# Optimization experiments

Hardware: AMD Instinct MI355X
Metric: run time of the kernel (lower is better)

The kernel has to match this reference:

```python
import jax, jax.numpy as jnp
import numpy as np
from jax import lax

PAD_TOKEN = 1
VOCAB = 32000
HID = 512
B, T, M = 32, 512, 6


def setup_inputs() -> dict:
    key = jax.random.key(0)
    ks = jax.random.split(key, 12)
    lim_g = 1.0 / np.sqrt(HID)
    lim_w = 1.0 / np.sqrt(2 * HID)
    u = lambda k, shape, lim: jax.random.uniform(k, shape, jnp.float32, -lim, lim)
    inp = {
        "input_seqs": jax.random.randint(ks[0], (B, T, M), 0, VOCAB, dtype=jnp.int32),
        "input_lengths": jax.random.randint(ks[1], (B,), 1, T + 1, dtype=jnp.int32),
        "emb": jax.random.normal(ks[2], (VOCAB, HID), jnp.float32),
        # forward GRU cell (Keras GRUCell, reset_after=True)
        "k_f": u(ks[3], (HID, 3 * HID), lim_g),
        "rk_f": u(ks[4], (HID, 3 * HID), lim_g),
        "b_f": u(ks[5], (2, 3 * HID), lim_g),
        # backward GRU cell
        "k_b": u(ks[6], (HID, 3 * HID), lim_g),
        "rk_b": u(ks[7], (HID, 3 * HID), lim_g),
        "b_b": u(ks[8], (2, 3 * HID), lim_g),
        # output projection W: 2H -> H
        "Wk": u(ks[9], (2 * HID, HID), lim_w),
        "Wb": u(ks[10], (HID,), lim_w),
    }
    return inp


def _gru_dir(x, mask, kernel, rkernel, bias, reverse):
    """Masked GRU scan. x: [B,T,H], mask: [B,T] bool. Keras GRUCell (reset_after=True).
    Masked timesteps carry previous state/output through (Keras semantics)."""
    b_in, b_rec = bias[0], bias[1]
    xs = x @ kernel + b_in                      # [B,T,3H], precompute input GEMM
    xs_t = jnp.swapaxes(xs, 0, 1)               # [T,B,3H]
    m_t = jnp.swapaxes(mask, 0, 1)              # [T,B]
    h0 = jnp.zeros((x.shape[0], rkernel.shape[0]), x.dtype)

    def step(h, inp):
        xt, mt = inp
        inner = h @ rkernel + b_rec             # [B,3H]
        xz, xr, xh = jnp.split(xt, 3, axis=-1)
        iz, ir, ih = jnp.split(inner, 3, axis=-1)
        z = jax.nn.sigmoid(xz + iz)
        r = jax.nn.sigmoid(xr + ir)
        hh = jnp.tanh(xh + r * ih)
        hn = z * h + (1.0 - z) * hh
        hn = jnp.where(mt[:, None], hn, h)      # masked step: carry state
        return hn, hn

    hT, outs = lax.scan(step, h0, (xs_t, m_t), reverse=reverse)
    return jnp.swapaxes(outs, 0, 1), hT         # [B,T,H], [B,H]


def reference(input_seqs, input_lengths, emb, k_f, rk_f, b_f, k_b, rk_b, b_b, Wk, Wb):
    # embedding lookup + PAD masking, sum over memory-tuple axis
    e = emb[input_seqs]                                       # [B,T,M,H]
    pad_mask = (input_seqs != PAD_TOKEN).astype(e.dtype)      # [B,T,M]
    embedded = jnp.sum(e * pad_mask[..., None], axis=2)       # [B,T,H]
    # (dropout p=0.0 -> identity)

    time_mask = jnp.arange(T)[None, :] < input_lengths[:, None]  # [B,T] bool

    out_f, h_f = _gru_dir(embedded, time_mask, k_f, rk_f, b_f, reverse=False)
    out_b, h_b = _gru_dir(embedded, time_mask, k_b, rk_b, b_b, reverse=True)

    outputs = jnp.concatenate([out_f, out_b], axis=-1)        # [B,T,2H]
    hidden_hat = jnp.concatenate([h_f, h_b], axis=-1)         # [B,2H]

    hidden = hidden_hat @ Wk + Wb                             # [B,H]
    outputs = outputs @ Wk + Wb                               # [B,T,H]
    return outputs, hidden
```

## Files before the change

### kernel.cpp

```cpp
#include <hip/hip_runtime.h>

typedef _Float16 f16;
typedef f16  f16x8 __attribute__((ext_vector_type(8)));
typedef float f32x4 __attribute__((ext_vector_type(4)));
typedef unsigned int u32;
typedef unsigned short u16;

#define NB   32
#define NT   512
#define NM   6
#define NH   512
#define NH3  1536
#define PADTOK 1
#define LO_SCALE 4096.0f
#define LO_INV   (1.0f/4096.0f)

#define XS2F_OFF  33685504
#define XS2B_OFF  100794368
#define HB_OFF    167903232
#define SLOT_STRIDE 544
#define FLAGS_U32 (2 * 32 * SLOT_STRIDE)
#define PLANE_E   16384

__device__ __forceinline__ void coh_store_u16(u16* base, u32 voff, u32 val) {
  asm volatile("global_store_short %0, %1, %2 sc0 sc1"
               :: "v"(voff), "v"(val), "s"(base) : "memory");
}

__global__ __launch_bounds__(128) void k_embed(const int* __restrict__ seqs,
                                               const float* __restrict__ emb,
                                               f16* __restrict__ Ahi,
                                               f16* __restrict__ Alo,
                                               f16* __restrict__ A2,
                                               u32* __restrict__ flags) {
  int row = blockIdx.x;
  int tid = threadIdx.x;
  if (row < 32) {
    for (int c2 = tid; c2 < 1024; c2 += 128)
      A2[(size_t)(16416 + row) * 1024 + c2] = (f16)0.f;
  }
  if (row < 64) {
    for (int j = row * 128 + tid; j < FLAGS_U32; j += 64 * 128)
      flags[j] = 0u;
  }
  const int* tr = seqs + (size_t)row * NM;
  int c0 = tid * 4;
  float acc0 = 0.f, acc1 = 0.f, acc2 = 0.f, acc3 = 0.f;
  for (int m = 0; m < NM; m++) {
    int tk = tr[m];
    if (tk != PADTOK) {
      float4 ev = *(const float4*)(emb + (size_t)tk * NH + c0);
      acc0 += ev.x; acc1 += ev.y; acc2 += ev.z; acc3 += ev.w;
    }
  }
  float a[4] = {acc0, acc1, acc2, acc3};
  for (int j = 0; j < 4; j++) {
    float v = a[j];
    f16 h = (f16)v;
    float lo = (v - (float)h) * LO_SCALE;
    Ahi[(size_t)row * NH + c0 + j] = h;
    Alo[(size_t)row * NH + c0 + j] = (f16)lo;
  }
}

__global__ __launch_bounds__(256) void k_gemm_in(const f16* __restrict__ Ahi,
                                                 const f16* __restrict__ Alo,
                                                 const float* __restrict__ Bw,
                                                 const float* __restrict__ bias,
                                                 f16* __restrict__ xs2) {
  __shared__ f16 BsH[64][40];
  __shared__ f16 BsL[64][40];
  int bx = blockIdx.x, by = blockIdx.y;
  int tid = threadIdx.x;
  int w = tid >> 6, l = tid & 63;
  int row0 = bx * 64 + w * 16;
  int col0 = by * 64;
  int arow = row0 + (l & 15);
  int kg = (l >> 4) * 8;
  f32x4 acc[4], accs[4];
  for (int nt = 0; nt < 4; nt++) {
    float bv = bias[col0 + nt * 16 + (l & 15)];
    f32x4 t = {bv, bv, bv, bv};
    acc[nt] = t;
    f32x4 z = {0.f, 0.f, 0.f, 0.f};
    accs[nt] = z;
  }
  for (int kb = 0; kb < NH; kb += 32) {
    __syncthreads();
    for (int idx = tid; idx < 2048; idx += 256) {
      int n = idx & 63, kl = idx >> 6;
      float v = Bw[(size_t)(kb + kl) * NH3 + col0 + n];
      f16 h = (f16)v;
      BsH[n][kl] = h;
      BsL[n][kl] = (f16)((v - (float)h) * LO_SCALE);
    }
    __syncthreads();
    f16x8 ah = *(const f16x8*)(Ahi + (size_t)arow * NH + kb + kg);
    f16x8 al = *(const f16x8*)(Alo + (size_t)arow * NH + kb + kg);
    for (int nt = 0; nt < 4; nt++) {
      f16x8 bh = *(const f16x8*)(&BsH[nt * 16 + (l & 15)][kg]);
      f16x8 bl = *(const f16x8*)(&BsL[nt * 16 + (l & 15)][kg]);
      acc[nt]  = __builtin_amdgcn_mfma_f32_16x16x32_f16(ah, bh, acc[nt], 0, 0, 0);
      accs[nt] = __builtin_amdgcn_mfma_f32_16x16x32_f16(al, bh, accs[nt], 0, 0, 0);
      accs[nt] = __builtin_amdgcn_mfma_f32_16x16x32_f16(ah, bl, accs[nt], 0, 0, 0);
    }
  }
  for (int nt = 0; nt < 4; nt++)
    for (int r = 0; r < 4; r++) {
      int grow = row0 + (l >> 4) * 4 + r;
      int b = grow >> 9, t = grow & (NT - 1);
      int gcol = col0 + nt * 16 + (l & 15);
      int g = gcol >> 9, u = gcol & 511;
      int ss = u >> 4, cc = u & 15;
      float v = acc[nt][r] + accs[nt][r] * LO_INV;
      f16 h = (f16)v;
      size_t idx = (size_t)(t * 32 + ss) * 2048 + g * 512 + b * 16 + cc;
      xs2[idx] = h;
      if (g == 2)
        xs2[idx + 512] = (f16)(v - (float)h);
    }
}

__global__ __launch_bounds__(128) void k_recur(const f16* __restrict__ xs2_f,
                                               const f16* __restrict__ xs2_b,
                                               const float* __restrict__ rk_f,
                                               const float* __restrict__ rk_b,
                                               const float* __restrict__ b_f,
                                               const float* __restrict__ b_b,
                                               const int* __restrict__ lens,
                                               u16* __restrict__ hb_f,
                                               u16* __restrict__ hb_b,
                                               f16* __restrict__ A2,
                                               u32* __restrict__ flags,
                                               int ring_mask) {
  __shared__ f16 WsH[48 * 512];
  __shared__ f16 WsL[48 * 512];
  int wg = blockIdx.x;
  int d = wg >> 5;
  int s = wg & 31;
  int u0 = s * 16;
  int tid = threadIdx.x;
  int w = tid >> 6, l = tid & 63;
  const f16*   xs2 = d ? xs2_b : xs2_f;
  u16*         myhb = d ? hb_b : hb_f;
  const float* rk = d ? rk_b : rk_f;
  const float* bb = d ? b_b  : b_f;

  for (int idx = tid; idx < 48 * 512; idx += 128) {
    int k = idx / 48, n = idx % 48;
    int gcol = (n >> 4) * NH + u0 + (n & 15);
    float v = rk[(size_t)k * NH3 + gcol];
    f16 h = (f16)v;
    f16 lo = (f16)((v - (float)h) * LO_SCALE);
    int byte = (n * 1024 + k * 2) ^ ((n & 7) << 4);
    *(f16*)((char*)WsH + byte) = h;
    *(f16*)((char*)WsL + byte) = lo;
  }
  __syncthreads();

  int c = l & 15;
  float brz = bb[NH3 + 0 * NH + u0 + c];
  float brr = bb[NH3 + 1 * NH + u0 + c];
  float brh = bb[NH3 + 2 * NH + u0 + c];
  int mrow[4], lenv[4];
  float hstate[4];
  u32 vo_h[4];
  for (int r = 0; r < 4; r++) {
    int b = w * 16 + (l >> 4) * 4 + r;
    mrow[r] = b;
    lenv[r] = lens[b];
    hstate[r] = 0.f;
    vo_h[r] = (u32)(s * 1024 + b * 32 + c * 2);
  }
  const int fbase = (d * 32 + s) * SLOT_STRIDE;
  for (int r = 0; r < 4; r++)
    coh_store_u16(myhb, vo_h[r], 0u);
  asm volatile("s_waitcnt vmcnt(0)" ::: "memory");
  __syncthreads();
  if (tid == 0)
    __hip_atomic_store(&flags[fbase + 0], 1u,
                       __ATOMIC_RELAXED, __HIP_MEMORY_SCOPE_AGENT);

  int arow_b = w * 16 + (l & 15);
  int kg = (l >> 4) * 8;
  int cbase = c * 1024;
  int zc = (c & 7) << 4;
  int hbase_lane = (kg >> 4) * 1024 + arow_b * 32 + (kg & 15) * 2;

#pragma unroll 1
  for (int i = 0; i < NT; i++) {
    int t = d ? (NT - 1 - i) : i;
    const u16* hplane = myhb + (size_t)(i & ring_mask) * PLANE_E;
    u16* wplane = myhb + (size_t)((i + 1) & ring_mask) * PLANE_E;

    if (tid < 32) {
      const u32* fp = flags + (d * 32 + tid) * SLOT_STRIDE + i;
      while (__hip_atomic_load(fp, __ATOMIC_RELAXED, __HIP_MEMORY_SCOPE_AGENT) == 0u)
        __builtin_amdgcn_s_sleep(1);
    }
    __syncthreads();

    const u16* sl = (const u16*)(xs2 + (size_t)(t * 32 + s) * 2048);
    u16 rxz[4], rxr[4], rxh[4], rxl[4];
#pragma unroll
    for (int r = 0; r < 4; r++) {
      int bo = mrow[r] * 16 + c;
      rxz[r] = sl[bo];
      rxr[r] = sl[512 + bo];
      rxh[r] = sl[1024 + bo];
      rxl[r] = sl[1536 + bo];
    }

    f32x4 a0, a1, a2, s0, s1, s2;
#pragma unroll
    for (int r = 0; r < 4; r++) {
      a0[r] = 0.f; a1[r] = 0.f; a2[r] = 0.f;
      s0[r] = 0.f; s1[r] = 0.f; s2[r] = 0.f;
    }
#pragma unroll
    for (int kk = 0; kk < 16; kk++) {
      f16x8 ah = *(const f16x8*)((const char*)hplane + hbase_lane + kk * 2048);
      int kb2 = (kk * 32 + kg) * 2;
      int off = (cbase + kb2) ^ zc;
      f16x8 b0h = *(const f16x8*)((const char*)WsH + off);
      f16x8 b1h = *(const f16x8*)((const char*)WsH + 16384 + off);
      f16x8 b2h = *(const f16x8*)((const char*)WsH + 32768 + off);
      f16x8 b0l = *(const f16x8*)((const char*)WsL + off);
      f16x8 b1l = *(const f16x8*)((const char*)WsL + 16384 + off);
      f16x8 b2l = *(const f16x8*)((const char*)WsL + 32768 + off);
      a0 = __builtin_amdgcn_mfma_f32_16x16x32_f16(ah, b0h, a0, 0, 0, 0);
      s0 = __builtin_amdgcn_mfma_f32_16x16x32_f16(ah, b0l, s0, 0, 0, 0);
      a1 = __builtin_amdgcn_mfma_f32_16x16x32_f16(ah, b1h, a1, 0, 0, 0);
      s1 = __builtin_amdgcn_mfma_f32_16x16x32_f16(ah, b1l, s1, 0, 0, 0);
      a2 = __builtin_amdgcn_mfma_f32_16x16x32_f16(ah, b2h, a2, 0, 0, 0);
      s2 = __builtin_amdgcn_mfma_f32_16x16x32_f16(ah, b2l, s2, 0, 0, 0);
    }

#pragma unroll
    for (int r = 0; r < 4; r++) {
      union { u16 u; f16 f; } uz, ur, uh, ul;
      uz.u = rxz[r]; ur.u = rxr[r]; uh.u = rxh[r]; ul.u = rxl[r];
      float az = a0[r] + s0[r] * LO_INV + (float)uz.f + brz;
      float ar = a1[r] + s1[r] * LO_INV + (float)ur.f + brr;
      float ahg = a2[r] + s2[r] * LO_INV;
      float xh = (float)uh.f + (float)ul.f;
      float z  = 1.f / (1.f + __expf(-az));
      float rr = 1.f / (1.f + __expf(-ar));
      float hh = tanhf(xh + rr * (ahg + brh));
      float hn = z * hstate[r] + (1.f - z) * hh;
      bool msk = t < lenv[r];
      hn = msk ? hn : hstate[r];
      hstate[r] = hn;
      union { f16 f; u16 u; } chv;
      chv.f = (f16)hn;
      coh_store_u16(wplane, vo_h[r], (u32)chv.u);
    }
    asm volatile("s_waitcnt vmcnt(0)" ::: "memory");
    __syncthreads();
    if (tid == 0)
      __hip_atomic_store(&flags[fbase + i + 1], 1u,
                         __ATOMIC_RELAXED, __HIP_MEMORY_SCOPE_AGENT);
#pragma unroll
    for (int r = 0; r < 4; r++)
      A2[((size_t)mrow[r] * NT + t) * 1024 + d * NH + u0 + c] = (f16)hstate[r];
  }
  for (int r = 0; r < 4; r++)
    A2[(size_t)(16384 + mrow[r]) * 1024 + d * NH + u0 + c] = (f16)hstate[r];
}

__global__ __launch_bounds__(256) void k_gemm_out(const f16* __restrict__ A2,
                                                  const float* __restrict__ Wk,
                                                  const float* __restrict__ Wb,
                                                  float* __restrict__ Out) {
  __shared__ f16 Bs[64][40];
  int bx = blockIdx.x, by = blockIdx.y;
  int tid = threadIdx.x;
  int w = tid >> 6, l = tid & 63;
  int row0 = bx * 64 + w * 16;
  int col0 = by * 64;
  int arow = row0 + (l & 15);
  int kg = (l >> 4) * 8;
  f32x4 acc[4];
  for (int nt = 0; nt < 4; nt++) {
    float bv = Wb[col0 + nt * 16 + (l & 15)];
    f32x4 t = {bv, bv, bv, bv};
    acc[nt] = t;
  }
  for (int kb = 0; kb < 1024; kb += 32) {
    __syncthreads();
    for (int idx = tid; idx < 2048; idx += 256) {
      int n = idx & 63, kl = idx >> 6;
      Bs[n][kl] = (f16)Wk[(size_t)(kb + kl) * NH + col0 + n];
    }
    __syncthreads();
    f16x8 av = *(const f16x8*)(A2 + (size_t)arow * 1024 + kb + kg);
    for (int nt = 0; nt < 4; nt++) {
      f16x8 bv = *(const f16x8*)(&Bs[nt * 16 + (l & 15)][kg]);
      acc[nt] = __builtin_amdgcn_mfma_f32_16x16x32_f16(av, bv, acc[nt], 0, 0, 0);
    }
  }
  for (int nt = 0; nt < 4; nt++)
    for (int r = 0; r < 4; r++) {
      int grow = row0 + (l >> 4) * 4 + r;
      if (grow < 16416)
        Out[(size_t)grow * NH + col0 + nt * 16 + (l & 15)] = acc[nt][r];
    }
}

extern "C" void kernel_launch(void* const* d_in, const int* in_sizes, int n_in,
                              void* d_out, int out_size, void* d_ws, size_t ws_size,
                              hipStream_t stream) {
  (void)in_sizes; (void)n_in; (void)out_size;
  const int*   seqs = (const int*)d_in[0];
  const int*   lens = (const int*)d_in[1];
  const float* emb  = (const float*)d_in[2];
  const float* k_f  = (const float*)d_in[3];
  const float* rk_f = (const float*)d_in[4];
  const float* b_f  = (const float*)d_in[5];
  const float* k_b  = (const float*)d_in[6];
  const float* rk_b = (const float*)d_in[7];
  const float* b_b  = (const float*)d_in[8];
  const float* Wk   = (const float*)d_in[9];
  const float* Wb   = (const float*)d_in[10];
  float* out = (float*)d_out;
  char* ws = (char*)d_ws;
  f16* A2     = (f16*)(ws + 0);
  f16* Ahi    = (f16*)(ws + 0);
  f16* Alo    = (f16*)(ws + 16777216);
  f16* xs2_f  = (f16*)(ws + XS2F_OFF);
  f16* xs2_b  = (f16*)(ws + XS2B_OFF);

  int ring = 512;
  size_t need512 = (size_t)HB_OFF + 2ull * 512 * 32768 + (size_t)FLAGS_U32 * 4;
  if (ws_size < need512) ring = 64;
  u16* hb_f = (u16*)(ws + HB_OFF);
  u16* hb_b = hb_f + (size_t)ring * PLANE_E;
  u32* flags = (u32*)(ws + HB_OFF + 2ull * ring * 32768);
  int ring_mask = ring - 1;

  hipLaunchKernelGGL(k_embed, dim3(16384), dim3(128), 0, stream, seqs, emb, Ahi, Alo, A2, flags);
  hipLaunchKernelGGL(k_gemm_in, dim3(256, 24), dim3(256), 0, stream, Ahi, Alo, k_f, b_f, xs2_f);
  hipLaunchKernelGGL(k_gemm_in, dim3(256, 24), dim3(256), 0, stream, Ahi, Alo, k_b, b_b, xs2_b);
  hipLaunchKernelGGL(k_recur, dim3(64), dim3(128), 0, stream,
                     xs2_f, xs2_b, rk_f, rk_b, b_f, b_b, lens, hb_f, hb_b, A2, flags, ring_mask);
  hipLaunchKernelGGL(k_gemm_out, dim3(257, 8), dim3(256), 0, stream, A2, Wk, Wb, out);
}
```

Baseline: 3.774 ms.

## Use per-wave flags and packed dword hidden-state stores in GRU recurrence

Each workgroup's two waves now signal and poll their own per-wave flags, which removes the block-level __syncthreads barriers from every timestep; the flag array doubles in size to hold them. Pairs of lanes now combine their f16 hidden values with a shuffle and write them as one coherent dword store instead of two short stores. This is meant to shorten the per-step critical path of the serial recurrence, at the cost of more flag polling traffic and a riskier memory-ordering scheme. Correctness relies on each wave reading only hidden rows written by the matching wave of the other workgroups.

Result: slower. 3.891 ms (+3.1%).

```diff
diff --git a/kernel.cpp b/kernel.cpp
--- a/kernel.cpp
+++ b/kernel.cpp
@@ -19,11 +19,11 @@
 #define XS2B_OFF  100794368
 #define HB_OFF    167903232
 #define SLOT_STRIDE 544
-#define FLAGS_U32 (2 * 32 * SLOT_STRIDE)
+#define FLAGS_U32 (2 * 32 * 2 * SLOT_STRIDE)
 #define PLANE_E   16384
 
-__device__ __forceinline__ void coh_store_u16(u16* base, u32 voff, u32 val) {
-  asm volatile("global_store_short %0, %1, %2 sc0 sc1"
+__device__ __forceinline__ void coh_store_u32(u32* base, u32 voff, u32 val) {
+  asm volatile("global_store_dword %0, %1, %2 sc0 sc1"
                :: "v"(voff), "v"(val), "s"(base) : "memory");
 }
 
@@ -140,7 +140,7 @@
   int s = wg & 31;
   int u0 = s * 16;
   int tid = threadIdx.x;
-  int w = tid >> 6, l = tid & 63;
+  int wv = tid >> 6, l = tid & 63;
   const f16*   xs2 = d ? xs2_b : xs2_f;
   u16*         myhb = d ? hb_b : hb_f;
   const float* rk = d ? rk_b : rk_f;
@@ -164,24 +164,24 @@
   float brh = bb[NH3 + 2 * NH + u0 + c];
   int mrow[4], lenv[4];
   float hstate[4];
-  u32 vo_h[4];
+  u32 vo32[4];
   for (int r = 0; r < 4; r++) {
-    int b = w * 16 + (l >> 4) * 4 + r;
+    int b = wv * 16 + (l >> 4) * 4 + r;
     mrow[r] = b;
     lenv[r] = lens[b];
     hstate[r] = 0.f;
-    vo_h[r] = (u32)(s * 1024 + b * 32 + c * 2);
-  }
-  const int fbase = (d * 32 + s) * SLOT_STRIDE;
+    vo32[r] = (u32)(s * 1024 + b * 32 + (c & ~1) * 2);
+  }
+  const int fbase = ((d * 32 + s) * 2 + wv) * SLOT_STRIDE;
   for (int r = 0; r < 4; r++)
-    coh_store_u16(myhb, vo_h[r], 0u);
+    if ((l & 1) == 0)
+      coh_store_u32((u32*)myhb, vo32[r], 0u);
   asm volatile("s_waitcnt vmcnt(0)" ::: "memory");
-  __syncthreads();
-  if (tid == 0)
+  if (l == 0)
     __hip_atomic_store(&flags[fbase + 0], 1u,
                        __ATOMIC_RELAXED, __HIP_MEMORY_SCOPE_AGENT);
 
-  int arow_b = w * 16 + (l & 15);
+  int arow_b = wv * 16 + (l & 15);
   int kg = (l >> 4) * 8;
   int cbase = c * 1024;
   int zc = (c & 7) << 4;
@@ -191,14 +191,14 @@
   for (int i = 0; i < NT; i++) {
     int t = d ? (NT - 1 - i) : i;
     const u16* hplane = myhb + (size_t)(i & ring_mask) * PLANE_E;
-    u16* wplane = myhb + (size_t)((i + 1) & ring_mask) * PLANE_E;
-
-    if (tid < 32) {
-      const u32* fp = flags + (d * 32 + tid) * SLOT_STRIDE + i;
+    u32* wplane32 = (u32*)(myhb + (size_t)((i + 1) & ring_mask) * PLANE_E);
+
+    if (l < 32) {
+      const u32* fp = flags + ((d * 32 + l) * 2 + wv) * SLOT_STRIDE + i;
       while (__hip_atomic_load(fp, __ATOMIC_RELAXED, __HIP_MEMORY_SCOPE_AGENT) == 0u)
         __builtin_amdgcn_s_sleep(1);
     }
-    __syncthreads();
+    asm volatile("" ::: "memory");
 
     const u16* sl = (const u16*)(xs2 + (size_t)(t * 32 + s) * 2048);
     u16 rxz[4], rxr[4], rxh[4], rxl[4];
@@ -236,6 +236,7 @@
       s2 = __builtin_amdgcn_mfma_f32_16x16x32_f16(ah, b2l, s2, 0, 0, 0);
     }
 
+    u16 hu[4];
 #pragma unroll
     for (int r = 0; r < 4; r++) {
       union { u16 u; f16 f; } uz, ur, uh, ul;
@@ -253,11 +254,16 @@
       hstate[r] = hn;
       union { f16 f; u16 u; } chv;
       chv.f = (f16)hn;
-      coh_store_u16(wplane, vo_h[r], (u32)chv.u);
+      hu[r] = chv.u;
+    }
+#pragma unroll
+    for (int r = 0; r < 4; r++) {
+      u32 other = (u32)__shfl_xor((int)hu[r], 1);
+      if ((l & 1) == 0)
+        coh_store_u32(wplane32, vo32[r], (u32)hu[r] | (other << 16));
     }
     asm volatile("s_waitcnt vmcnt(0)" ::: "memory");
-    __syncthreads();
-    if (tid == 0)
+    if (l == 0)
       __hip_atomic_store(&flags[fbase + i + 1], 1u,
                          __ATOMIC_RELAXED, __HIP_MEMORY_SCOPE_AGENT);
 #pragma unroll
```
